# Kernel optimization log

Hardware: AMD Instinct MI355X
Metric: run time of the kernel (lower is better)

Reference implementation:

```python
import jax, jax.numpy as jnp
import numpy as np

T, B, E, H, DFF, K = 1024, 4, 512, 8, 2048, 31
D = E // H  # head_dim


def double_swish(x):
    # DoubleSwish: x * sigmoid(x - 1)
    return x * jax.nn.sigmoid(x - 1.0)


def ffn(x, w1, b1, w2, b2):
    # ScaledLinear -> ActivationBalancer(identity in eval) -> DoubleSwish -> ScaledLinear
    return double_swish(x @ w1.T + b1) @ w2.T + b2


def rel_shift(x):
    # x: (B, H, T, 2T-1) -> (B, H, T, T); out[b,h,i,j] = x[b,h,i, (T-1) - i + j]
    t = x.shape[2]
    idx = (t - 1) - jnp.arange(t)[:, None] + jnp.arange(t)[None, :]  # (T, T)
    return jnp.take_along_axis(x, idx[None, None], axis=-1)


def self_attn(x, pos_emb, wqkv, bqkv, wo, bo, wpos, u, v):
    # x: (T, B, E); Transformer-XL style rel-pos multi-head attention
    t, b, e = x.shape
    qkv = x @ wqkv.T + bqkv                       # (T, B, 3E)
    q, k, val = jnp.split(qkv, 3, axis=-1)
    q = q * (D ** -0.5)
    to_heads = lambda z: z.reshape(t, b, H, D).transpose(1, 2, 0, 3)  # (B,H,T,D)
    q, k, val = to_heads(q), to_heads(k), to_heads(val)
    # positional projection: (1, 2T-1, E) -> (1, H, D, 2T-1)
    p = (pos_emb @ wpos.T).reshape(1, 2 * t - 1, H, D).transpose(0, 2, 3, 1)
    ac = jnp.einsum('bhld,bhsd->bhls', q + u[None, :, None, :], k)
    bd = jnp.einsum('bhld,bhdm->bhlm', q + v[None, :, None, :], p)
    scores = ac + rel_shift(bd)                   # (B, H, T, T)
    attn = jax.nn.softmax(scores, axis=-1)
    out = jnp.einsum('bhls,bhsd->bhld', attn, val)
    out = out.transpose(2, 0, 1, 3).reshape(t, b, e)  # (T, B, E)
    return out @ wo.T + bo


def conv_module(x, pw1_w, pw1_b, dw_w, dw_b, pw2_w, pw2_b):
    # x: (T, B, C) -> (B, C, T)
    x = x.transpose(1, 2, 0)
    x = jnp.einsum('oc,bct->bot', pw1_w, x) + pw1_b[None, :, None]  # (B, 2C, T)
    a, g = jnp.split(x, 2, axis=1)
    x = a * jax.nn.sigmoid(g)                     # GLU over channel dim
    pad = (K - 1) // 2
    x = jax.lax.conv_general_dilated(
        x, dw_w, window_strides=(1,), padding=[(pad, pad)],
        dimension_numbers=('NCH', 'OIH', 'NCH'), feature_group_count=E)
    x = double_swish(x + dw_b[None, :, None])
    x = jnp.einsum('oc,bct->bot', pw2_w, x) + pw2_b[None, :, None]
    return x.transpose(2, 0, 1)                   # (T, B, C)


def basic_norm(x, log_eps):
    # BasicNorm: x * (mean(x^2, -1) + exp(eps))^{-0.5}
    return x * jax.lax.rsqrt(jnp.mean(x * x, axis=-1, keepdims=True) + jnp.exp(log_eps))


def setup_inputs() -> dict:
    key = jax.random.key(0)
    ks = jax.random.split(key, 24)
    std = jnp.float32(0.02)
    f = lambda k, s: jax.random.normal(k, s, jnp.float32)
    return dict(
        src=f(ks[0], (T, B, E)),
        pos_emb=f(ks[1], (1, 2 * T - 1, E)),
        in_proj_w=f(ks[2], (3 * E, E)) * std,
        in_proj_b=f(ks[3], (3 * E,)) * std,
        out_proj_w=f(ks[4], (E, E)) * std,
        out_proj_b=f(ks[5], (E,)) * std,
        linear_pos_w=f(ks[6], (E, E)) * std,
        pos_bias_u=f(ks[7], (H, D)) * jnp.float32(0.01),
        pos_bias_v=f(ks[8], (H, D)) * jnp.float32(0.01),
        ffm_w1=f(ks[9], (DFF, E)) * std, ffm_b1=f(ks[10], (DFF,)) * std,
        ffm_w2=f(ks[11], (E, DFF)) * std, ffm_b2=f(ks[12], (E,)) * std,
        ff_w1=f(ks[13], (DFF, E)) * std, ff_b1=f(ks[14], (DFF,)) * std,
        ff_w2=f(ks[15], (E, DFF)) * std, ff_b2=f(ks[16], (E,)) * std,
        conv_pw1_w=f(ks[17], (2 * E, E)) * std, conv_pw1_b=f(ks[18], (2 * E,)) * std,
        conv_dw_w=f(ks[19], (E, 1, K)) * std, conv_dw_b=f(ks[20], (E,)) * std,
        conv_pw2_w=f(ks[21], (E, E)) * std, conv_pw2_b=f(ks[22], (E,)) * std,
        norm_eps=jnp.array(np.log(0.25), jnp.float32),
    )


def reference(src, pos_emb, in_proj_w, in_proj_b, out_proj_w, out_proj_b,
              linear_pos_w, pos_bias_u, pos_bias_v,
              ffm_w1, ffm_b1, ffm_w2, ffm_b2,
              ff_w1, ff_b1, ff_w2, ff_b2,
              conv_pw1_w, conv_pw1_b, conv_dw_w, conv_dw_b, conv_pw2_w, conv_pw2_b,
              norm_eps):
    # macaron FFN
    x = src + ffn(src, ffm_w1, ffm_b1, ffm_w2, ffm_b2)
    # rel-pos self-attention
    x = x + self_attn(x, pos_emb, in_proj_w, in_proj_b, out_proj_w, out_proj_b,
                      linear_pos_w, pos_bias_u, pos_bias_v)
    # convolution module
    x = x + conv_module(x, conv_pw1_w, conv_pw1_b, conv_dw_w, conv_dw_b, conv_pw2_w, conv_pw2_b)
    # second FFN
    x = x + ffn(x, ff_w1, ff_b1, ff_w2, ff_b2)
    # balancer is identity in eval; final BasicNorm
    return basic_norm(x, norm_eps)
```

## Files before the change

kernel.cpp:

```cpp
#include <hip/hip_runtime.h>
#include <string.h>


#define T_ 1024
#define B_ 4
#define E_ 512
#define H_ 8
#define DFF_ 2048
#define KW_ 31

typedef unsigned short u16;
typedef unsigned int u32;
typedef __bf16 bf16x8 __attribute__((ext_vector_type(8)));
typedef float floatx4 __attribute__((ext_vector_type(4)));

__device__ __forceinline__ float b2f(u16 u) {
    return __uint_as_float(((u32)u) << 16);
}
__device__ __forceinline__ u16 f2b(float f) {
    u32 i = __float_as_uint(f);
    u32 r = (i + 0x7fffu + ((i >> 16) & 1u)) >> 16;
    return (u16)r;
}

__device__ __forceinline__ void glds16(const u16 *g, u16 *l) {
    __builtin_amdgcn_global_load_lds((const __attribute__((address_space(1))) void *)g,
                                     (__attribute__((address_space(3))) void *)l, 16, 0, 0);
}

__global__ __launch_bounds__(256) void fill_k(float *out, long long n, float val) {
    long long g = (long long)blockIdx.x * 256 + threadIdx.x;
    if (g < n) out[g] = val;
}

__global__ __launch_bounds__(256) void detect_k(const u16 *src16, int *flag) {
    __shared__ int sh[256];
    int tid = threadIdx.x;
    int cnt = 0;
    for (int i = tid; i < 4096; i += 256) {
        u16 x = src16[2 * i];
        int e = (x >> 7) & 0xFF;
        cnt += (e == 0 || (e >= 0x70 && e <= 0x8F)) ? 1 : 0;
    }
    sh[tid] = cnt;
    __syncthreads();
    for (int s = 128; s; s >>= 1) {
        if (tid < s) sh[tid] += sh[tid + s];
        __syncthreads();
    }
    if (tid == 0) *flag = (sh[0] < 2048) ? 1 : 0;
}

struct CVT {
    const void *in[24];
    long long pre[25];
};

__global__ __launch_bounds__(256) void convert_k(CVT c, u16 *dst, const int *flag,
                                                 long long total) {
    long long g = (long long)blockIdx.x * 256 + threadIdx.x;
    if (g >= total) return;
    int s = 0;
#pragma unroll
    for (int i = 1; i < 25; i++) s += (g >= c.pre[i]) ? 1 : 0;
    long long l = g - c.pre[s];
    int f = *flag;
    u16 v = f ? f2b(((const float *)c.in[s])[l]) : ((const u16 *)c.in[s])[l];
    dst[g] = v;
}

struct GP {
    const u16 *A, *B;
    u16 *C;
    const u16 *bias;
    const void *resin;
    float *xr;
    u16 *xb;
    const u16 *ub, *vb;
    u16 *qu, *qv, *kh, *vt;
    int M, N, K, lda, ldb, ldc, mode, qcols, resin_f32;
    float qscale;
};

__global__ __launch_bounds__(512) void gemm_nt(GP p) {
    __shared__ __align__(16) u16 As[4 * 4096];
    __shared__ __align__(16) u16 Bs[4 * 4096];
    const int tid = threadIdx.x;
    const int wv = tid >> 6, ln = tid & 63;
    const int l16 = ln & 15, quad = ln >> 4;
    const int wm = (wv >> 2) << 5;
    const int wn = (wv & 3) << 4;
    const int gx = gridDim.x;
    const int nb = gx * gridDim.y;
    const int lid = blockIdx.y * gx + blockIdx.x;
    const int nid = (lid & 7) * (nb >> 3) + (lid >> 3);
    const int m0 = (nid / gx) << 6, n0 = (nid % gx) << 6;
    floatx4 zero = {0.f, 0.f, 0.f, 0.f};
    floatx4 acc[2];
    acc[0] = zero;
    acc[1] = zero;

    const int NT = p.K >> 6;

    const int srow = tid >> 3;
    const int sg = ((tid & 7) ^ (srow & 7)) << 3;
    int ra = m0 + srow;
    if (ra > p.M - 1) ra = p.M - 1;
    const u16 *Agp = p.A + (long long)ra * p.lda + sg;
    const u16 *Bgp = p.B + (long long)(n0 + srow) * p.ldb + sg;

    auto stage = [&](int bidx, int t) {
        const int k0 = t << 6;
        const int o = bidx << 12;
        glds16(Agp + k0, As + o + tid * 8);
        glds16(Bgp + k0, Bs + o + tid * 8);
    };
    auto compute = [&](int bidx) {
        const int o = bidx << 12;
#pragma unroll
        for (int kk = 0; kk < 2; kk++) {
            const int swz = ((((kk << 2) | quad) ^ (l16 & 7)) << 3);
            bf16x8 bfv = __builtin_bit_cast(bf16x8,
                *(const uint4 *)&Bs[o + ((wn + l16) << 6) + swz]);
#pragma unroll
            for (int mt = 0; mt < 2; mt++) {
                bf16x8 af = __builtin_bit_cast(bf16x8,
                    *(const uint4 *)&As[o + ((wm + (mt << 4) + l16) << 6) + swz]);
                acc[mt] = __builtin_amdgcn_mfma_f32_16x16x32_bf16(af, bfv, acc[mt], 0, 0, 0);
            }
        }
    };

    stage(0, 0);
    stage(1, 1);
    stage(2, 2);
    stage(3, 3);
    asm volatile("s_waitcnt vmcnt(4)" ::: "memory");
    __builtin_amdgcn_s_barrier();

    const int NP = NT >> 1;
    for (int ph = 0; ph < NP; ph++) {
        const int b0 = (ph << 1) & 3;
        compute(b0);
        compute(b0 | 1);
        if (ph + 1 < NP) {
            __builtin_amdgcn_sched_barrier(0);
            __builtin_amdgcn_s_barrier();
            if (ph + 2 < NP) {
                stage(b0, (ph << 1) + 4);
                stage(b0 | 1, (ph << 1) + 5);
                asm volatile("s_waitcnt vmcnt(4)" ::: "memory");
            } else {
                asm volatile("s_waitcnt vmcnt(0)" ::: "memory");
            }
            __builtin_amdgcn_s_barrier();
            __builtin_amdgcn_sched_barrier(0);
        }
    }

#pragma unroll
    for (int mt = 0; mt < 2; mt++) {
#pragma unroll
        for (int r = 0; r < 4; r++) {
            int gr = m0 + wm + (mt << 4) + (quad << 2) + r;
            int gc = n0 + wn + l16;
            bool oob = gr >= p.M;
            if (oob && p.mode != 3) continue;
            float y = 0.f;
            if (!oob) {
                y = acc[mt][r];
                if (p.bias) y += b2f(p.bias[gc]);
                if (gc < p.qcols) y *= p.qscale;
            }
            if (p.mode == 3) {
                p.C[((gc >> 6) << 17) + (gr << 6) + (gc & 63)] = f2b(y);
            } else if (p.mode == 0) {
                p.C[(long long)gr * p.ldc + gc] = f2b(y);
            } else if (p.mode == 1) {
                float s = 1.f / (1.f + __expf(1.f - y));
                p.C[(long long)gr * p.ldc + gc] = f2b(y * s);
            } else {
                long long idx = (long long)gr * p.ldc + gc;
                float rv = p.resin_f32 ? ((const float *)p.resin)[idx]
                                       : b2f(((const u16 *)p.resin)[idx]);
                float o = rv + y;
                p.xr[idx] = o;
                if (p.xb) p.xb[idx] = f2b(o);
            }
        }
    }
}

__global__ __launch_bounds__(512) void gemm_nt128(GP p) {
    __shared__ __align__(16) u16 As[4 * 4096];
    __shared__ __align__(16) u16 Bs[4 * 4096];
    const int tid = threadIdx.x;
    const int wv = tid >> 6, ln = tid & 63;
    const int l16 = ln & 15, quad = ln >> 4;
    const int wm = (wv >> 2) << 6;
    const int wn = (wv & 3) << 5;
    const int gx = gridDim.x;
    const int nb = gx * gridDim.y;
    const int lid = blockIdx.y * gx + blockIdx.x;
    const int nid = (lid & 7) * (nb >> 3) + (lid >> 3);
    const int m0 = (nid / gx) << 7, n0 = (nid % gx) << 7;
    const int srow = tid >> 2;
    const int sg = ((tid & 3) ^ ((tid >> 3) & 3)) << 3;
    const u16 *Agp = p.A + (long long)(m0 + srow) * p.lda + sg;
    const u16 *Bgp = p.B + (long long)(n0 + srow) * p.ldb + sg;
    floatx4 zero = {0.f, 0.f, 0.f, 0.f};
    floatx4 acc[4][2];
#pragma unroll
    for (int i = 0; i < 4; i++)
#pragma unroll
        for (int j = 0; j < 2; j++) acc[i][j] = zero;

    const int rswz = ((quad ^ ((l16 >> 1) & 3)) << 3);
    const int NT = p.K >> 5;

    auto stage = [&](int bidx, int t) {
        const int k0 = t << 5;
        const int o = bidx << 12;
        glds16(Agp + k0, As + o + tid * 8);
        glds16(Bgp + k0, Bs + o + tid * 8);
    };
    auto compute = [&](int bidx) {
        const int o = bidx << 12;
        bf16x8 av[4], bv[2];
#pragma unroll
        for (int mt = 0; mt < 4; mt++)
            av[mt] = __builtin_bit_cast(bf16x8,
                *(const uint4 *)&As[o + ((wm + (mt << 4) + l16) << 5) + rswz]);
#pragma unroll
        for (int nt = 0; nt < 2; nt++)
            bv[nt] = __builtin_bit_cast(bf16x8,
                *(const uint4 *)&Bs[o + ((wn + (nt << 4) + l16) << 5) + rswz]);
#pragma unroll
        for (int mt = 0; mt < 4; mt++)
#pragma unroll
            for (int nt = 0; nt < 2; nt++)
                acc[mt][nt] = __builtin_amdgcn_mfma_f32_16x16x32_bf16(av[mt], bv[nt],
                                                                      acc[mt][nt], 0, 0, 0);
    };

    stage(0, 0);
    stage(1, 1);
    stage(2, 2);
    stage(3, 3);
    asm volatile("s_waitcnt vmcnt(4)" ::: "memory");
    __builtin_amdgcn_s_barrier();

    const int NP = NT >> 1;
    for (int ph = 0; ph < NP; ph++) {
        const int b0 = (ph << 1) & 3;
        compute(b0);
        compute(b0 | 1);
        if (ph + 1 < NP) {
            __builtin_amdgcn_sched_barrier(0);
            __builtin_amdgcn_s_barrier();
            if (ph + 2 < NP) {
                stage(b0, (ph << 1) + 4);
                stage(b0 | 1, (ph << 1) + 5);
                asm volatile("s_waitcnt vmcnt(4)" ::: "memory");
            } else {
                asm volatile("s_waitcnt vmcnt(0)" ::: "memory");
            }
            __builtin_amdgcn_s_barrier();
            __builtin_amdgcn_sched_barrier(0);
        }
    }

#pragma unroll
    for (int mt = 0; mt < 4; mt++)
#pragma unroll
        for (int nt = 0; nt < 2; nt++)
#pragma unroll
            for (int r = 0; r < 4; r++) {
                int gr = m0 + wm + (mt << 4) + (quad << 2) + r;
                int gc = n0 + wn + (nt << 4) + l16;
                float y = acc[mt][nt][r];
                if (p.bias) y += b2f(p.bias[gc]);
                if (gc < p.qcols) y *= p.qscale;
                if (p.mode == 0) {
                    p.C[(long long)gr * p.ldc + gc] = f2b(y);
                } else if (p.mode == 1) {
                    float s = 1.f / (1.f + __expf(1.f - y));
                    p.C[(long long)gr * p.ldc + gc] = f2b(y * s);
                } else if (p.mode == 4) {
                    int t = gr >> 2, b = gr & 3;
                    if (gc < E_) {
                        int z = b * 8 + (gc >> 6);
                        long long oq = ((long long)z << 16) + (t << 6) + (gc & 63);
                        p.qu[oq] = f2b(y + b2f(p.ub[gc]));
                        p.qv[oq] = f2b(y + b2f(p.vb[gc]));
                    } else if (gc < 2 * E_) {
                        int c = gc - E_;
                        int z = b * 8 + (c >> 6);
                        p.kh[((long long)z << 16) + (t << 6) + (c & 63)] = f2b(y);
                    } else {
                        int c = gc - 2 * E_;
                        int z = b * 8 + (c >> 6);
                        p.vt[(long long)((z << 6) + (c & 63)) * T_ + t] = f2b(y);
                    }
                } else {
                    long long idx = (long long)gr * p.ldc + gc;
                    float rv = p.resin_f32 ? ((const float *)p.resin)[idx]
                                           : b2f(((const u16 *)p.resin)[idx]);
                    float o = rv + y;
                    p.xr[idx] = o;
                    if (p.xb) p.xb[idx] = f2b(o);
                }
            }
}

__global__ __launch_bounds__(512) void gemm_glu(const u16 *A, const u16 *W, const u16 *bias,
                                                u16 *ch) {
    __shared__ __align__(16) u16 As[3 * 4096];
    __shared__ __align__(16) u16 Ba[3 * 4096];
    __shared__ __align__(16) u16 Bg[3 * 4096];
    const int tid = threadIdx.x;
    const int wv = tid >> 6, ln = tid & 63;
    const int l16 = ln & 15, quad = ln >> 4;
    const int wm = (wv >> 2) << 5;
    const int wn = (wv & 3) << 4;
    const int gx = gridDim.x;
    const int nb = gx * gridDim.y;
    const int lid = blockIdx.y * gx + blockIdx.x;
    const int nid = (lid & 7) * (nb >> 3) + (lid >> 3);
    const int m0 = (nid / gx) << 6, n0 = (nid % gx) << 6;
    floatx4 zero = {0.f, 0.f, 0.f, 0.f};
    floatx4 aa[2], ag[2];
    aa[0] = zero; aa[1] = zero; ag[0] = zero; ag[1] = zero;

    const int NT = 8;
    const int srow = tid >> 3;
    const int sg = ((tid & 7) ^ (srow & 7)) << 3;
    const u16 *Agp = A + ((long long)(m0 + srow) << 9) + sg;
    const u16 *Bap = W + ((long long)(n0 + srow) << 9) + sg;
    const u16 *Bgp = W + ((long long)(E_ + n0 + srow) << 9) + sg;

    auto stage = [&](int bidx, int t) {
        const int k0 = t << 6;
        const int o = bidx << 12;
        glds16(Agp + k0, As + o + tid * 8);
        glds16(Bap + k0, Ba + o + tid * 8);
        glds16(Bgp + k0, Bg + o + tid * 8);
    };

    stage(0, 0);
    stage(1, 1);
    stage(2, 2);
    asm volatile("s_waitcnt vmcnt(6)" ::: "memory");
    __builtin_amdgcn_s_barrier();

    int cb = 0;
    for (int t = 0; t < NT; t++) {
        const int o = cb << 12;
#pragma unroll
        for (int kk = 0; kk < 2; kk++) {
            const int swz = ((((kk << 2) | quad) ^ (l16 & 7)) << 3);
            bf16x8 ba = __builtin_bit_cast(bf16x8,
                *(const uint4 *)&Ba[o + ((wn + l16) << 6) + swz]);
            bf16x8 bg = __builtin_bit_cast(bf16x8,
                *(const uint4 *)&Bg[o + ((wn + l16) << 6) + swz]);
#pragma unroll
            for (int mt = 0; mt < 2; mt++) {
                bf16x8 af = __builtin_bit_cast(bf16x8,
                    *(const uint4 *)&As[o + ((wm + (mt << 4) + l16) << 6) + swz]);
                aa[mt] = __builtin_amdgcn_mfma_f32_16x16x32_bf16(af, ba, aa[mt], 0, 0, 0);
                ag[mt] = __builtin_amdgcn_mfma_f32_16x16x32_bf16(af, bg, ag[mt], 0, 0, 0);
            }
        }
        if (t + 1 < NT) {
            __builtin_amdgcn_sched_barrier(0);
            __builtin_amdgcn_s_barrier();
            if (t + 3 < NT) {
                stage(cb, t + 3);
                asm volatile("s_waitcnt vmcnt(6)" ::: "memory");
            } else if (t + 2 < NT) {
                asm volatile("s_waitcnt vmcnt(3)" ::: "memory");
            } else {
                asm volatile("s_waitcnt vmcnt(0)" ::: "memory");
            }
            __builtin_amdgcn_s_barrier();
            __builtin_amdgcn_sched_barrier(0);
        }
        cb = (cb == 2) ? 0 : cb + 1;
    }

#pragma unroll
    for (int mt = 0; mt < 2; mt++) {
#pragma unroll
        for (int r = 0; r < 4; r++) {
            int gr = m0 + wm + (mt << 4) + (quad << 2) + r;
            int gc = n0 + wn + l16;
            float a = aa[mt][r] + b2f(bias[gc]);
            float g = ag[mt][r] + b2f(bias[E_ + gc]);
            ch[((long long)gr << 9) + gc] = f2b(a * (1.f / (1.f + __expf(-g))));
        }
    }
}

struct FK {
    const u16 *QU, *QV, *KH, *PPH, *VT;
    u16 *attno;
};

__global__ __launch_bounds__(256) void flash_k(FK p) {
    __shared__ __align__(16) u16 lds[2 * 16384 + 4608];

    const int tid = threadIdx.x;
    const int wv = tid >> 6, ln = tid & 63;
    const int l16 = ln & 15, quad = ln >> 4;
    const int lid = blockIdx.y * 16 + blockIdx.x;
    const int nid = (lid & 7) * 64 + (lid >> 3);
    const int zg = nid >> 4;
    const int i0 = (nid & 15) << 6;
    const u16 *kh0 = p.KH + (long long)zg * 65536;
    const u16 *ph0 = p.PPH + (long long)(zg & 7) * 131072;
    const u16 *vt0 = p.VT + (long long)zg * 65536;
    u16 *Pb = lds + 32768;

    auto stage = [&](int buf, int jt) {
        const int j0 = jt << 6;
        const int m_start = 960 - i0 + j0;
        u16 *Kh = lds + (buf << 14);
        u16 *Vt = Kh + 4096;
        u16 *Ph = Kh + 8192;
#pragma unroll
        for (int ps = 0; ps < 2; ps++) {
            int g = ps * 256 + tid;
            int row = g >> 3;
            int src = ((g & 7) ^ (row & 7)) << 3;
            glds16(kh0 + ((j0 + row) << 6) + src, Kh + g * 8);
            glds16(vt0 + (row << 10) + j0 + src, Vt + g * 8);
        }
#pragma unroll
        for (int ps = 0; ps < 4; ps++) {
            int g = ps * 256 + tid;
            int row = g >> 3;
            int src = ((g & 7) ^ (row & 7)) << 3;
            glds16(ph0 + ((m_start + row) << 6) + src, Ph + g * 8);
        }
    };

    const long long qoff = (long long)zg * 65536 + (long long)(i0 + (wv << 4) + l16) * 64 + (quad << 3);
    bf16x8 aqu[2], aqv[2];
#pragma unroll
    for (int kk = 0; kk < 2; kk++) {
        aqu[kk] = __builtin_bit_cast(bf16x8, *(const uint4 *)(p.QU + qoff + (kk << 5)));
        aqv[kk] = __builtin_bit_cast(bf16x8, *(const uint4 *)(p.QV + qoff + (kk << 5)));
    }

    stage(0, 0);
    asm volatile("s_waitcnt vmcnt(0)" ::: "memory");
    __builtin_amdgcn_s_barrier();

    float lacc[4];
    floatx4 accO[4];
    floatx4 zero = {0.f, 0.f, 0.f, 0.f};
#pragma unroll
    for (int e = 0; e < 4; e++) lacc[e] = 0.f;
#pragma unroll
    for (int i = 0; i < 4; i++) accO[i] = zero;

    const int r16q = quad << 2;

    for (int jt = 0; jt < 16; jt++) {
        if (jt + 1 < 16) stage((jt + 1) & 1, jt + 1);
        __builtin_amdgcn_sched_barrier(0);
        const int o = (jt & 1) << 14;
        const u16 *Kh = lds + o;
        const u16 *Vt = lds + o + 4096;
        const u16 *Ph = lds + o + 8192;

        floatx4 aS[4], aB[5];
#pragma unroll
        for (int i = 0; i < 4; i++) aS[i] = zero;
#pragma unroll
        for (int i = 0; i < 5; i++) aB[i] = zero;
        __builtin_amdgcn_s_setprio(1);
#pragma unroll
        for (int kk = 0; kk < 2; kk++) {
            const int swz = ((((kk << 2) | quad) ^ (l16 & 7)) << 3);
#pragma unroll
            for (int nt = 0; nt < 4; nt++) {
                bf16x8 bf = __builtin_bit_cast(bf16x8,
                    *(const uint4 *)&Kh[(((nt << 4) | l16) << 6) + swz]);
                aS[nt] = __builtin_amdgcn_mfma_f32_16x16x32_bf16(aqu[kk], bf, aS[nt], 0, 0, 0);
            }
#pragma unroll
            for (int rt = 0; rt < 5; rt++) {
                bf16x8 bf = __builtin_bit_cast(bf16x8,
                    *(const uint4 *)&Ph[((((rt + 3 - wv) << 4) | l16) << 6) + swz]);
                aB[rt] = __builtin_amdgcn_mfma_f32_16x16x32_bf16(aqv[kk], bf, aB[rt], 0, 0, 0);
            }
        }
        __builtin_amdgcn_s_setprio(0);

#pragma unroll
        for (int e = 0; e < 4; e++) {
            const int r16 = r16q + e;
            const int t = l16 + 15 - r16;
            const int srcl = (quad << 4) | (t & 15);
            const int carry = t >> 4;
            float ps = 0.f;
#pragma unroll
            for (int nt = 0; nt < 4; nt++) {
                float vlo = __shfl(aB[nt][e], srcl, 64);
                float vhi = __shfl(aB[nt + 1][e], srcl, 64);
                float bd = carry ? vhi : vlo;
                float pe = __expf(aS[nt][e] + bd);
                ps += pe;
                Pb[(((wv << 4) + r16) * 72) + (nt << 4) + l16] = f2b(pe);
            }
            lacc[e] += ps;
        }

        __builtin_amdgcn_s_setprio(1);
#pragma unroll
        for (int kk = 0; kk < 2; kk++) {
            const int swz = ((((kk << 2) | quad) ^ (l16 & 7)) << 3);
            bf16x8 ap = __builtin_bit_cast(bf16x8,
                *(const uint4 *)&Pb[(((wv << 4) | l16) * 72) + (kk << 5) + (quad << 3)]);
#pragma unroll
            for (int nd = 0; nd < 4; nd++) {
                bf16x8 bv = __builtin_bit_cast(bf16x8,
                    *(const uint4 *)&Vt[(((nd << 4) | l16) << 6) + swz]);
                accO[nd] = __builtin_amdgcn_mfma_f32_16x16x32_bf16(ap, bv, accO[nd], 0, 0, 0);
            }
        }
        __builtin_amdgcn_s_setprio(0);

        if (jt + 1 < 16) {
            __builtin_amdgcn_sched_barrier(0);
            __builtin_amdgcn_s_barrier();
            asm volatile("s_waitcnt vmcnt(0)" ::: "memory");
            __builtin_amdgcn_s_barrier();
            __builtin_amdgcn_sched_barrier(0);
        }
    }

    const int b = zg >> 3, h = zg & 7;
#pragma unroll
    for (int e = 0; e < 4; e++) {
#pragma unroll
        for (int msk = 1; msk < 16; msk <<= 1) lacc[e] += __shfl_xor(lacc[e], msk, 64);
        float inv = 1.f / lacc[e];
        int t = i0 + (wv << 4) + (quad << 2) + e;
#pragma unroll
        for (int nd = 0; nd < 4; nd++) {
            int d = (nd << 4) + l16;
            p.attno[(long long)(t * B_ + b) * E_ + h * 64 + d] = f2b(accO[nd][e] * inv);
        }
    }
}


__global__ __launch_bounds__(256) void dwconv_k(const u16 *ch, const u16 *w, const u16 *bias,
                                                u16 *cd) {
    const int cp = threadIdx.x;
    const int b = blockIdx.x >> 7;
    const int t0 = (blockIdx.x & 127) << 3;
    const int c0 = cp << 1;
    float in0[38], in1[38];
#pragma unroll
    for (int j = 0; j < 38; j++) {
        int tt = t0 - 15 + j;
        u32 v = 0;
        if (tt >= 0 && tt < T_) v = *(const u32 *)&ch[tt * 2048 + b * 512 + c0];
        in0[j] = b2f((u16)(v & 0xffff));
        in1[j] = b2f((u16)(v >> 16));
    }
    float w0[KW_], w1[KW_];
#pragma unroll
    for (int kk = 0; kk < KW_; kk++) {
        w0[kk] = b2f(w[c0 * KW_ + kk]);
        w1[kk] = b2f(w[c0 * KW_ + KW_ + kk]);
    }
    float bi0 = b2f(bias[c0]), bi1 = b2f(bias[c0 + 1]);
#pragma unroll
    for (int t = 0; t < 8; t++) {
        float a0 = bi0, a1 = bi1;
#pragma unroll
        for (int kk = 0; kk < KW_; kk++) {
            a0 += in0[t + kk] * w0[kk];
            a1 += in1[t + kk] * w1[kk];
        }
        float s0 = 1.f / (1.f + __expf(1.f - a0));
        float s1 = 1.f / (1.f + __expf(1.f - a1));
        u32 o = (u32)f2b(a0 * s0) | ((u32)f2b(a1 * s1) << 16);
        *(u32 *)&cd[(t0 + t) * 2048 + b * 512 + c0] = o;
    }
}

__global__ __launch_bounds__(256) void norm_k(const float *xr, const float *epsp, float *out) {
    int wv = threadIdx.x >> 6, ln = threadIdx.x & 63;
    long long row = blockIdx.x * 4 + wv;
    const float *x = xr + row * E_;
    float vals[8], ss = 0.f;
#pragma unroll
    for (int i = 0; i < 8; i++) {
        vals[i] = x[ln + (i << 6)];
        ss += vals[i] * vals[i];
    }
#pragma unroll
    for (int m = 32; m; m >>= 1) ss += __shfl_xor(ss, m, 64);
    float sc = rsqrtf(ss * (1.f / (float)E_) + __expf(epsp[0]));
    float *o = out + row * E_;
#pragma unroll
    for (int i = 0; i < 8; i++) o[ln + (i << 6)] = vals[i] * sc;
}


extern "C" void kernel_launch(void *const *d_in, const int *in_sizes, int n_in,
                              void *d_out, int out_size, void *d_ws, size_t ws_size,
                              hipStream_t stream) {
    const size_t MB = (size_t)1 << 20;
    static const long long EXPECT[24] = {
        2097152, 1048064, 786432, 1536, 262144, 512, 262144, 512, 512,
        1048576, 2048, 1048576, 512, 1048576, 2048, 1048576, 512,
        524288, 1024, 15872, 512, 262144, 512, 1};
    const size_t NEED = 93 * MB;

    float code = 0.f;
    if (n_in != 24) {
        code = 1000.f + (float)n_in;
    } else {
        for (int i = 0; i < 24; i++) {
            if ((long long)in_sizes[i] != EXPECT[i]) { code = 2000.f + 64.f * i; break; }
        }
    }
    if (code == 0.f && out_size != 2097152) code = 3000.f;
    if (code == 0.f && ws_size < NEED) code = 5000.f + (float)(ws_size / MB);
    if (code != 0.f) {
        long long n = (long long)out_size;
        fill_k<<<dim3((unsigned)((n + 255) / 256)), dim3(256), 0, stream>>>((float *)d_out, n, code);
        return;
    }

    char *w = (char *)d_ws;
    int *flag = (int *)(w + 0);
    u16 *cv = (u16 *)(w + 1 * MB);
    float *xr = (float *)(w + 21 * MB);
    u16 *xb = (u16 *)(w + 29 * MB);
    u16 *h1 = (u16 *)(w + 33 * MB);
    u16 *pph = (u16 *)(w + 63 * MB);
    u16 *QU = (u16 *)(w + 65 * MB);
    u16 *QV = (u16 *)(w + 69 * MB);
    u16 *KH = (u16 *)(w + 73 * MB);
    u16 *VT = (u16 *)(w + 77 * MB);
    u16 *attno = (u16 *)(w + 81 * MB);
    u16 *ch = (u16 *)(w + 85 * MB);
    u16 *cd = (u16 *)(w + 89 * MB);

    detect_k<<<dim3(1), dim3(256), 0, stream>>>((const u16 *)d_in[0], flag);
    CVT c;
    c.pre[0] = 0;
    for (int i = 0; i < 24; i++) {
        c.in[i] = d_in[i];
        c.pre[i + 1] = c.pre[i] + in_sizes[i];
    }
    long long total = c.pre[24];
    convert_k<<<dim3((unsigned)((total + 255) / 256)), dim3(256), 0, stream>>>(c, cv, flag, total);

    const u16 *src = cv + c.pre[0];
    const u16 *pos_emb = cv + c.pre[1];
    const u16 *w_qkv = cv + c.pre[2];
    const u16 *b_qkv = cv + c.pre[3];
    const u16 *w_o = cv + c.pre[4];
    const u16 *b_o = cv + c.pre[5];
    const u16 *w_pos = cv + c.pre[6];
    const u16 *u_bias = cv + c.pre[7];
    const u16 *v_bias = cv + c.pre[8];
    const u16 *ffm_w1 = cv + c.pre[9];
    const u16 *ffm_b1 = cv + c.pre[10];
    const u16 *ffm_w2 = cv + c.pre[11];
    const u16 *ffm_b2 = cv + c.pre[12];
    const u16 *ff_w1 = cv + c.pre[13];
    const u16 *ff_b1 = cv + c.pre[14];
    const u16 *ff_w2 = cv + c.pre[15];
    const u16 *ff_b2 = cv + c.pre[16];
    const u16 *pw1_w = cv + c.pre[17];
    const u16 *pw1_b = cv + c.pre[18];
    const u16 *dw_w = cv + c.pre[19];
    const u16 *dw_b = cv + c.pre[20];
    const u16 *pw2_w = cv + c.pre[21];
    const u16 *pw2_b = cv + c.pre[22];

    auto mk = [](const void *A, int lda, const void *B, int ldb, void *C, int ldc,
                 const void *bias, int M, int N, int K, int mode) {
        GP p;
        memset(&p, 0, sizeof(p));
        p.A = (const u16 *)A; p.B = (const u16 *)B; p.C = (u16 *)C; p.bias = (const u16 *)bias;
        p.M = M; p.N = N; p.K = K; p.lda = lda; p.ldb = ldb; p.ldc = ldc; p.mode = mode;
        p.qscale = 1.f;
        return p;
    };
    auto launch = [&](GP p) {
        dim3 g((p.N + 63) / 64, (p.M + 63) / 64, 1);
        gemm_nt<<<g, dim3(512), 0, stream>>>(p);
    };
    auto launch128 = [&](GP p) {
        dim3 g(p.N >> 7, p.M >> 7, 1);
        gemm_nt128<<<g, dim3(512), 0, stream>>>(p);
    };

    const int M = T_ * B_;

    { GP p = mk(src, E_, ffm_w1, E_, h1, DFF_, ffm_b1, M, DFF_, E_, 1); launch128(p); }
    { GP p = mk(h1, DFF_, ffm_w2, DFF_, nullptr, E_, ffm_b2, M, E_, DFF_, 2);
      p.resin = d_in[0]; p.resin_f32 = 1; p.xr = xr; p.xb = xb; launch(p); }

    { GP p = mk(xb, E_, w_qkv, E_, nullptr, 3 * E_, b_qkv, M, 3 * E_, E_, 4);
      p.qcols = E_; p.qscale = 0.125f;
      p.ub = u_bias; p.vb = v_bias; p.qu = QU; p.qv = QV; p.kh = KH; p.vt = VT;
      launch128(p); }
    { GP p = mk(pos_emb, E_, w_pos, E_, pph, E_, nullptr, 2 * T_ - 1, E_, E_, 3); launch(p); }

    {
        FK f;
        f.QU = QU; f.QV = QV; f.KH = KH; f.PPH = pph; f.VT = VT; f.attno = attno;
        flash_k<<<dim3(16, 32), dim3(256), 0, stream>>>(f);
    }

    { GP p = mk(attno, E_, w_o, E_, nullptr, E_, b_o, M, E_, E_, 2);
      p.resin = xr; p.resin_f32 = 1; p.xr = xr; p.xb = xb; launch(p); }

    gemm_glu<<<dim3(8, 64), dim3(512), 0, stream>>>(xb, pw1_w, pw1_b, ch);
    dwconv_k<<<dim3(512), dim3(256), 0, stream>>>(ch, dw_w, dw_b, cd);
    { GP p = mk(cd, E_, pw2_w, E_, nullptr, E_, pw2_b, M, E_, E_, 2);
      p.resin = xr; p.resin_f32 = 1; p.xr = xr; p.xb = xb; launch(p); }

    { GP p = mk(xb, E_, ff_w1, E_, h1, DFF_, ff_b1, M, DFF_, E_, 1); launch128(p); }
    { GP p = mk(h1, DFF_, ff_w2, DFF_, nullptr, E_, ff_b2, M, E_, DFF_, 2);
      p.resin = xr; p.resin_f32 = 1; p.xr = xr; p.xb = nullptr; launch(p); }

    norm_k<<<dim3(M / 4), dim3(256), 0, stream>>>(xr, (const float *)d_in[23], (float *)d_out);
}
```

Measured before the change: 351.8 us.

## Load LDS fragments to registers first and overlap next-stage global loads with MFMA

In both GEMM kernels, each phase now reads all LDS fragments for the two buffers into registers, waits on lgkmcnt, and then barriers. Only after that does it issue the async global-to-LDS loads for the next stages, before running the MFMA work. The aim is to overlap global memory traffic with matrix math instead of serializing compute and then staging. The cost is higher register pressure, since fragments for two buffers are held at once, and a changed barrier placement that has to keep buffer reuse correct.

```diff
diff --git a/kernel.cpp b/kernel.cpp
--- a/kernel.cpp
+++ b/kernel.cpp
@@ -115,20 +115,26 @@
         glds16(Agp + k0, As + o + tid * 8);
         glds16(Bgp + k0, Bs + o + tid * 8);
     };
-    auto compute = [&](int bidx) {
+    auto ldregs = [&](int bidx, bf16x8 *af, bf16x8 *bv) {
         const int o = bidx << 12;
 #pragma unroll
         for (int kk = 0; kk < 2; kk++) {
             const int swz = ((((kk << 2) | quad) ^ (l16 & 7)) << 3);
-            bf16x8 bfv = __builtin_bit_cast(bf16x8,
+            bv[kk] = __builtin_bit_cast(bf16x8,
                 *(const uint4 *)&Bs[o + ((wn + l16) << 6) + swz]);
 #pragma unroll
-            for (int mt = 0; mt < 2; mt++) {
-                bf16x8 af = __builtin_bit_cast(bf16x8,
+            for (int mt = 0; mt < 2; mt++)
+                af[kk * 2 + mt] = __builtin_bit_cast(bf16x8,
                     *(const uint4 *)&As[o + ((wm + (mt << 4) + l16) << 6) + swz]);
-                acc[mt] = __builtin_amdgcn_mfma_f32_16x16x32_bf16(af, bfv, acc[mt], 0, 0, 0);
-            }
-        }
+        }
+    };
+    auto mma = [&](const bf16x8 *af, const bf16x8 *bv) {
+#pragma unroll
+        for (int kk = 0; kk < 2; kk++)
+#pragma unroll
+            for (int mt = 0; mt < 2; mt++)
+                acc[mt] = __builtin_amdgcn_mfma_f32_16x16x32_bf16(af[kk * 2 + mt], bv[kk],
+                                                                  acc[mt], 0, 0, 0);
     };
 
     stage(0, 0);
@@ -141,14 +147,23 @@
     const int NP = NT >> 1;
     for (int ph = 0; ph < NP; ph++) {
         const int b0 = (ph << 1) & 3;
-        compute(b0);
-        compute(b0 | 1);
+        bf16x8 af0[4], bv0[2], af1[4], bv1[2];
+        ldregs(b0, af0, bv0);
+        ldregs(b0 | 1, af1, bv1);
+        __builtin_amdgcn_sched_barrier(0);
+        asm volatile("s_waitcnt lgkmcnt(0)" ::: "memory");
+        __builtin_amdgcn_s_barrier();
+        __builtin_amdgcn_sched_barrier(0);
+        const bool do_stage = (ph + 2 < NP);
+        if (do_stage) {
+            stage(b0, (ph << 1) + 4);
+            stage(b0 | 1, (ph << 1) + 5);
+        }
+        mma(af0, bv0);
+        mma(af1, bv1);
         if (ph + 1 < NP) {
             __builtin_amdgcn_sched_barrier(0);
-            __builtin_amdgcn_s_barrier();
-            if (ph + 2 < NP) {
-                stage(b0, (ph << 1) + 4);
-                stage(b0 | 1, (ph << 1) + 5);
+            if (do_stage) {
                 asm volatile("s_waitcnt vmcnt(4)" ::: "memory");
             } else {
                 asm volatile("s_waitcnt vmcnt(0)" ::: "memory");
@@ -224,9 +239,8 @@
         glds16(Agp + k0, As + o + tid * 8);
         glds16(Bgp + k0, Bs + o + tid * 8);
     };
-    auto compute = [&](int bidx) {
+    auto ldregs = [&](int bidx, bf16x8 *av, bf16x8 *bv) {
         const int o = bidx << 12;
-        bf16x8 av[4], bv[2];
 #pragma unroll
         for (int mt = 0; mt < 4; mt++)
             av[mt] = __builtin_bit_cast(bf16x8,
@@ -235,6 +249,8 @@
         for (int nt = 0; nt < 2; nt++)
             bv[nt] = __builtin_bit_cast(bf16x8,
                 *(const uint4 *)&Bs[o + ((wn + (nt << 4) + l16) << 5) + rswz]);
+    };
+    auto mma = [&](const bf16x8 *av, const bf16x8 *bv) {
 #pragma unroll
         for (int mt = 0; mt < 4; mt++)
 #pragma unroll
@@ -253,14 +269,23 @@
     const int NP = NT >> 1;
     for (int ph = 0; ph < NP; ph++) {
         const int b0 = (ph << 1) & 3;
-        compute(b0);
-        compute(b0 | 1);
+        bf16x8 av0[4], bv0[2], av1[4], bv1[2];
+        ldregs(b0, av0, bv0);
+        ldregs(b0 | 1, av1, bv1);
+        __builtin_amdgcn_sched_barrier(0);
+        asm volatile("s_waitcnt lgkmcnt(0)" ::: "memory");
+        __builtin_amdgcn_s_barrier();
+        __builtin_amdgcn_sched_barrier(0);
+        const bool do_stage = (ph + 2 < NP);
+        if (do_stage) {
+            stage(b0, (ph << 1) + 4);
+            stage(b0 | 1, (ph << 1) + 5);
+        }
+        mma(av0, bv0);
+        mma(av1, bv1);
         if (ph + 1 < NP) {
             __builtin_amdgcn_sched_barrier(0);
-            __builtin_amdgcn_s_barrier();
-            if (ph + 2 < NP) {
-                stage(b0, (ph << 1) + 4);
-                stage(b0 | 1, (ph << 1) + 5);
+            if (do_stage) {
                 asm volatile("s_waitcnt vmcnt(4)" ::: "memory");
             } else {
                 asm volatile("s_waitcnt vmcnt(0)" ::: "memory");
```

Measured after the change: 344.0 us. 2.2% less time.
